# Kernel optimization log

Measured on AMD Instinct MI355X. Metric: run time of the kernel, lower is better.

Reference implementation:

```python
import jax, jax.numpy as jnp
import numpy as np

WS = 8
NUM_HEADS = 8
EMBED_DIM = 256
LN_EPS = 1e-5


def setup_inputs() -> dict:
    key = jax.random.key(0)
    ks = jax.random.split(key, 5)
    b, c, h, w = 4, EMBED_DIM, 128, 128
    return {
        "x": jax.random.normal(ks[0], (b, c, h, w), dtype=jnp.float32),
        "in_proj_w": jax.random.normal(ks[1], (3 * c, c), dtype=jnp.float32) * 0.02,
        "in_proj_b": jax.random.normal(ks[2], (3 * c,), dtype=jnp.float32) * 0.02,
        "out_w": jax.random.normal(ks[3], (c, c), dtype=jnp.float32) * 0.02,
        "out_b": jax.random.normal(ks[4], (c,), dtype=jnp.float32) * 0.02,
        "ln_w": jnp.ones((c,), dtype=jnp.float32),
        "ln_b": jnp.zeros((c,), dtype=jnp.float32),
    }


def reference(x, in_proj_w, in_proj_b, out_w, out_b, ln_w, ln_b):
    b, c, h, w = x.shape
    pad_h = (-h) % WS
    pad_w = (-w) % WS
    xp = jnp.pad(x, ((0, 0), (0, 0), (0, pad_h), (0, pad_w)))
    Hp, Wp = h + pad_h, w + pad_w
    h1, w1 = Hp // WS, Wp // WS
    L = h1 * w1            # attention sequence = number of windows
    N = b * WS * WS        # attention batch = b * within-window positions
    # rearrange 'b c (h1 h2) (w1 w2) -> (h1 w1) (b h2 w2) c', then batch-first
    t = xp.reshape(b, c, h1, WS, w1, WS)
    t = jnp.transpose(t, (2, 4, 0, 3, 5, 1)).reshape(L, N, c)
    t = jnp.transpose(t, (1, 0, 2))  # [N, L, c]
    # nn.MultiheadAttention (self-attention, no mask)
    qkv = t @ in_proj_w.T + in_proj_b  # [N, L, 3c]
    q, k, v = jnp.split(qkv, 3, axis=-1)
    D = c // NUM_HEADS
    q = q.reshape(N, L, NUM_HEADS, D) * (D ** -0.5)
    k = k.reshape(N, L, NUM_HEADS, D)
    v = v.reshape(N, L, NUM_HEADS, D)
    attn = jax.nn.softmax(jnp.einsum('nlhd,nmhd->nhlm', q, k), axis=-1)
    o = jnp.einsum('nhlm,nmhd->nlhd', attn, v).reshape(N, L, c)
    o = o @ out_w.T + out_b
    # LayerNorm over channel dim
    mu = jnp.mean(o, axis=-1, keepdims=True)
    var = jnp.mean(jnp.square(o - mu), axis=-1, keepdims=True)
    o = (o - mu) * jax.lax.rsqrt(var + LN_EPS) * ln_w + ln_b
    # inverse rearrange '(h1 w1) (b h2 w2) c -> b c (h1 h2) (w1 w2)'
    y = jnp.transpose(o, (1, 0, 2)).reshape(h1, w1, b, WS, WS, c)
    y = jnp.transpose(y, (2, 5, 0, 3, 1, 4)).reshape(b, c, Hp, Wp)
    return y[:, :, :h, :w]
```

## Files before the change

kernel.cpp:

```cpp
#include <hip/hip_runtime.h>
#include <stdint.h>
#include <stddef.h>


typedef __attribute__((ext_vector_type(8))) short bf16x8;
typedef __attribute__((ext_vector_type(4))) float f32x4;
typedef __attribute__((ext_vector_type(16))) float f32x16;
typedef __attribute__((ext_vector_type(4))) unsigned u32x4;
typedef unsigned short bf16u;

#define LOG2E 1.4426950408889634f
#define MFMA32(a, b, c) __builtin_amdgcn_mfma_f32_32x32x16_bf16(a, b, c, 0, 0, 0)

__device__ __forceinline__ bf16u f2b(float f) {
  uint32_t u = __float_as_uint(f);
  u += 0x7fffu + ((u >> 16) & 1u);
  return (bf16u)(u >> 16);
}
__device__ __forceinline__ float b2f(bf16u s) {
  return __uint_as_float(((uint32_t)s) << 16);
}

__device__ __forceinline__ void gload_lds16(const void* g, void* l) {
  __builtin_amdgcn_global_load_lds((__attribute__((address_space(1))) void*)(g),
                                   (__attribute__((address_space(3))) void*)(l),
                                   16, 0, 0);
}

__device__ __forceinline__ unsigned cvtpk(float a, float b) {
  unsigned r;
  asm("v_cvt_pk_bf16_f32 %0, %1, %2" : "=v"(r) : "v"(a), "v"(b));
  return r;
}

__device__ __forceinline__ void swap32(unsigned a, unsigned b, bool hi,
                                       unsigned& x, unsigned& y) {
#if __has_builtin(__builtin_amdgcn_permlane32_swap)
  typedef __attribute__((ext_vector_type(2))) unsigned uint2v;
  uint2v r = __builtin_amdgcn_permlane32_swap(a, b, false, false);
  x = r.x;
  y = r.y;
#else
  unsigned as = (unsigned)__shfl_xor((int)a, 32);
  unsigned bs = (unsigned)__shfl_xor((int)b, 32);
  x = hi ? bs : a;
  y = hi ? b : as;
#endif
}

__global__ __launch_bounds__(256) void k_convert(const float* __restrict__ s,
                                                 bf16u* __restrict__ d, int n) {
  int i = blockIdx.x * 256 + threadIdx.x;
  if (i < n) d[i] = f2b(s[i]);
}

__global__ __launch_bounds__(256) void k_rearrange(const float* __restrict__ x,
                                                   bf16u* __restrict__ Tb) {
  const int bid = blockIdx.x;
  const int ct = bid & 7, hh = (bid >> 3) & 127, b = bid >> 10;
  const int c0 = ct * 32;
  const int h1 = hh >> 3, h2 = hh & 7;
  __shared__ float tile[32][129];
  for (int e = threadIdx.x; e < 4096; e += 256) {
    int cc = e >> 7, ww = e & 127;
    tile[cc][ww] = x[(((size_t)(b * 256 + c0 + cc)) * 128 + hh) * 128 + ww];
  }
  __syncthreads();
  for (int e = threadIdx.x; e < 4096; e += 256) {
    int ww = e >> 5, cc = e & 31;
    int w1 = ww >> 3, w2 = ww & 7;
    int i = ((b * 64 + h2 * 8 + w2) << 8) | (h1 * 16 + w1);
    Tb[(size_t)i * 256 + c0 + cc] = f2b(tile[cc][ww]);
  }
}

__global__ __launch_bounds__(256) void k_qkv(const bf16u* __restrict__ Tb,
                                             const bf16u* __restrict__ Wb,
                                             const float* __restrict__ bias,
                                             bf16u* __restrict__ Qb,
                                             bf16u* __restrict__ Kb,
                                             bf16u* __restrict__ Vtb) {
  __shared__ bf16u As[128 * 32];
  __shared__ bf16u Bs[128 * 32];
  const int bid0 = blockIdx.x;
  const int bid = (bid0 & 7) * 384 + (bid0 >> 3);
  const int o0 = (bid % 6) * 128;
  const int i0 = (bid / 6) * 128;
  const int seg = o0 >> 8;
  const int t = threadIdx.x;
  const int lane = t & 63, lo = lane & 15, hi = lane >> 4;
  const int w = t >> 6, wr = w >> 1, wc = w & 1;
  const int srow = t >> 2, schunk = (t & 3) * 8, sbase = (t & 192) * 8;
  f32x4 acc[4][4] = {};
  for (int k0 = 0; k0 < 256; k0 += 32) {
    __syncthreads();
    gload_lds16(Tb + (size_t)(i0 + srow) * 256 + k0 + schunk, As + sbase);
    gload_lds16(Tb + (size_t)(i0 + 64 + srow) * 256 + k0 + schunk, As + 2048 + sbase);
    gload_lds16(Wb + (size_t)(o0 + srow) * 256 + k0 + schunk, Bs + sbase);
    gload_lds16(Wb + (size_t)(o0 + 64 + srow) * 256 + k0 + schunk, Bs + 2048 + sbase);
    __syncthreads();
    bf16x8 af[4], bf_[4];
#pragma unroll
    for (int m = 0; m < 4; ++m)
      af[m] = *(const bf16x8*)&As[(wr * 64 + m * 16 + lo) * 32 + hi * 8];
#pragma unroll
    for (int nn = 0; nn < 4; ++nn)
      bf_[nn] = *(const bf16x8*)&Bs[(wc * 64 + nn * 16 + lo) * 32 + hi * 8];
#pragma unroll
    for (int m = 0; m < 4; ++m)
#pragma unroll
      for (int nn = 0; nn < 4; ++nn)
        acc[m][nn] = __builtin_amdgcn_mfma_f32_16x16x32_bf16(af[m], bf_[nn], acc[m][nn], 0, 0, 0);
  }
  const float oscale = (seg == 0) ? (0.17677669529663687f * LOG2E) : 1.0f;
  bf16u* const dst = (seg == 0) ? Qb : (seg == 1 ? Kb : Vtb);
#pragma unroll
  for (int m = 0; m < 4; ++m) {
#pragma unroll
    for (int nn = 0; nn < 4; ++nn) {
      const int o = o0 + wc * 64 + nn * 16 + lo;
      const int within = o & 255, head = within >> 5, dd = within & 31;
      const float bia = bias[o];
#pragma unroll
      for (int r = 0; r < 4; ++r) {
        int tok = i0 + wr * 64 + m * 16 + hi * 4 + r;
        float v = (acc[m][nn][r] + bia) * oscale;
        int nt = tok >> 8, ls = tok & 255;
        size_t idx;
        if (seg == 2)
          idx = ((size_t)((nt * 8 + head) * 32 + dd)) * 256 + ls;
        else
          idx = ((size_t)((nt * 8 + head) * 256 + ls)) * 32 + dd;
        dst[idx] = f2b(v);
      }
    }
  }
}

__global__ __launch_bounds__(256, 2) void k_attn(const bf16u* __restrict__ Qb,
                                                 const bf16u* __restrict__ Kb,
                                                 const bf16u* __restrict__ Vtb,
                                                 bf16u* __restrict__ Ob) {
  const int nh = blockIdx.x;
  const int n = nh >> 3, h = nh & 7;
  const bf16u* Qp = Qb + (size_t)nh * 8192;
  const bf16u* Kp = Kb + (size_t)nh * 8192;
  const bf16u* Vp = Vtb + (size_t)nh * 8192;
  const int t = threadIdx.x, w = t >> 6, lane = t & 63;
  const int l31 = lane & 31;
  const bool hi5 = (lane & 32) != 0;

  bf16x8 qf[2][2];
#pragma unroll
  for (int qs = 0; qs < 2; ++qs)
#pragma unroll
    for (int dh = 0; dh < 2; ++dh)
      qf[qs][dh] = *(const bf16x8*)(Qp + (size_t)(w * 64 + qs * 32 + l31) * 32 +
                                    dh * 16 + (hi5 ? 8 : 0));

  const bf16u* kbase = Kp + (size_t)l31 * 32 + (hi5 ? 8 : 0);
  const bf16u* vbase = Vp + (size_t)l31 * 256 + (hi5 ? 8 : 0);

  bf16x8 kf0 = *(const bf16x8*)(kbase);
  bf16x8 kf1 = *(const bf16x8*)(kbase + 16);
  bf16x8 vf0 = *(const bf16x8*)(vbase);
  bf16x8 vf1 = *(const bf16x8*)(vbase + 16);

  f32x16 accO[2] = {};
  float rsum[2] = {0.f, 0.f};

#pragma unroll
  for (int kt = 0; kt < 8; ++kt) {
    const int nkt = (kt + 1) & 7;
    bf16x8 nk0 = *(const bf16x8*)(kbase + nkt * 1024);
    bf16x8 nk1 = *(const bf16x8*)(kbase + nkt * 1024 + 16);
    bf16x8 nv0 = *(const bf16x8*)(vbase + nkt * 32);
    bf16x8 nv1 = *(const bf16x8*)(vbase + nkt * 32 + 16);

#pragma unroll
    for (int qs = 0; qs < 2; ++qs) {
      f32x16 s = {};
      s = MFMA32(kf0, qf[qs][0], s);
      s = MFMA32(kf1, qf[qs][1], s);
      float ts0 = 0.f, ts1 = 0.f;
      unsigned pk[8];
#pragma unroll
      for (int jp = 0; jp < 8; ++jp) {
        float p0 = exp2f(s[2 * jp]);
        float p1 = exp2f(s[2 * jp + 1]);
        ts0 += p0;
        ts1 += p1;
        pk[jp] = cvtpk(p0, p1);
      }
      float ts = ts0 + ts1;
      ts += __shfl_xor(ts, 32);
      rsum[qs] += ts;
      unsigned x0, x1, x2, x3, y0, y1, y2, y3;
      swap32(pk[0], pk[2], hi5, x0, x2);
      swap32(pk[1], pk[3], hi5, x1, x3);
      swap32(pk[4], pk[6], hi5, y0, y2);
      swap32(pk[5], pk[7], hi5, y1, y3);
      u32x4 pa0 = {x0, x1, x2, x3};
      u32x4 pa1 = {y0, y1, y2, y3};
      accO[qs] = MFMA32(__builtin_bit_cast(bf16x8, pa0), vf0, accO[qs]);
      accO[qs] = MFMA32(__builtin_bit_cast(bf16x8, pa1), vf1, accO[qs]);
    }
    kf0 = nk0;
    kf1 = nk1;
    vf0 = nv0;
    vf1 = nv1;
  }
#pragma unroll
  for (int qs = 0; qs < 2; ++qs) {
    float rn = 1.0f / rsum[qs];
#pragma unroll
    for (int r = 0; r < 16; ++r) {
      int row = (r & 3) + 8 * (r >> 2) + ((lane & 32) >> 3);
      float c = __shfl(rn, (lane & 32) | row);
      float o = accO[qs][r] * c;
      Ob[((size_t)(n * 256 + w * 64 + qs * 32 + row)) * 256 + h * 32 + l31] = f2b(o);
    }
  }
}

__global__ __launch_bounds__(256) void k_out(const bf16u* __restrict__ Ob,
                                             const bf16u* __restrict__ Wb,
                                             const float* __restrict__ bias,
                                             const float* __restrict__ lnw,
                                             const float* __restrict__ lnb,
                                             bf16u* __restrict__ On) {
  __shared__ bf16u As[64 * 32];
  __shared__ bf16u Bs[256 * 32];
  __shared__ float red[64][4][2];
  const int i0 = blockIdx.x * 64;
  const int t = threadIdx.x, w = t >> 6, lane = t & 63, lo = lane & 15, hi = lane >> 4;
  const int srow = t >> 2, schunk = (t & 3) * 8, sbase = (t & 192) * 8;
  f32x4 acc[4][4] = {};
  for (int k0 = 0; k0 < 256; k0 += 32) {
    __syncthreads();
    gload_lds16(Ob + (size_t)(i0 + srow) * 256 + k0 + schunk, As + sbase);
#pragma unroll
    for (int j = 0; j < 4; ++j)
      gload_lds16(Wb + (size_t)(j * 64 + srow) * 256 + k0 + schunk, Bs + j * 2048 + sbase);
    __syncthreads();
    bf16x8 af[4], bf_[4];
#pragma unroll
    for (int m = 0; m < 4; ++m)
      af[m] = *(const bf16x8*)&As[(m * 16 + lo) * 32 + hi * 8];
#pragma unroll
    for (int nn = 0; nn < 4; ++nn)
      bf_[nn] = *(const bf16x8*)&Bs[(w * 64 + nn * 16 + lo) * 32 + hi * 8];
#pragma unroll
    for (int m = 0; m < 4; ++m)
#pragma unroll
      for (int nn = 0; nn < 4; ++nn)
        acc[m][nn] = __builtin_amdgcn_mfma_f32_16x16x32_bf16(af[m], bf_[nn], acc[m][nn], 0, 0, 0);
  }
#pragma unroll
  for (int m = 0; m < 4; ++m)
#pragma unroll
    for (int nn = 0; nn < 4; ++nn) {
      float bia = bias[w * 64 + nn * 16 + lo];
#pragma unroll
      for (int r = 0; r < 4; ++r) acc[m][nn][r] += bia;
    }
#pragma unroll
  for (int m = 0; m < 4; ++m)
#pragma unroll
    for (int r = 0; r < 4; ++r) {
      float sv = acc[m][0][r] + acc[m][1][r] + acc[m][2][r] + acc[m][3][r];
      float sq = acc[m][0][r] * acc[m][0][r] + acc[m][1][r] * acc[m][1][r] +
                 acc[m][2][r] * acc[m][2][r] + acc[m][3][r] * acc[m][3][r];
      sv += __shfl_xor(sv, 1); sq += __shfl_xor(sq, 1);
      sv += __shfl_xor(sv, 2); sq += __shfl_xor(sq, 2);
      sv += __shfl_xor(sv, 4); sq += __shfl_xor(sq, 4);
      sv += __shfl_xor(sv, 8); sq += __shfl_xor(sq, 8);
      if (lo == 0) {
        red[m * 16 + hi * 4 + r][w][0] = sv;
        red[m * 16 + hi * 4 + r][w][1] = sq;
      }
    }
  __syncthreads();
#pragma unroll
  for (int m = 0; m < 4; ++m)
#pragma unroll
    for (int r = 0; r < 4; ++r) {
      int row = m * 16 + hi * 4 + r;
      float S  = red[row][0][0] + red[row][1][0] + red[row][2][0] + red[row][3][0];
      float Q2 = red[row][0][1] + red[row][1][1] + red[row][2][1] + red[row][3][1];
      float mu = S * 0.00390625f;
      float var = Q2 * 0.00390625f - mu * mu;
      float rstd = rsqrtf(var + 1e-5f);
#pragma unroll
      for (int nn = 0; nn < 4; ++nn) {
        int oc = w * 64 + nn * 16 + lo;
        float o = (acc[m][nn][r] - mu) * rstd * lnw[oc] + lnb[oc];
        On[(size_t)(i0 + row) * 256 + oc] = f2b(o);
      }
    }
}

__global__ __launch_bounds__(256) void k_unrearrange(const bf16u* __restrict__ On,
                                                     float* __restrict__ y) {
  const int bid = blockIdx.x;
  const int ct = bid & 7, hh = (bid >> 3) & 127, b = bid >> 10;
  const int c0 = ct * 32;
  const int h1 = hh >> 3, h2 = hh & 7;
  __shared__ float tile[32][129];
  for (int e = threadIdx.x; e < 4096; e += 256) {
    int ww = e >> 5, cc = e & 31;
    int w1 = ww >> 3, w2 = ww & 7;
    int i = ((b * 64 + h2 * 8 + w2) << 8) | (h1 * 16 + w1);
    tile[cc][ww] = b2f(On[(size_t)i * 256 + c0 + cc]);
  }
  __syncthreads();
  for (int e = threadIdx.x; e < 4096; e += 256) {
    int cc = e >> 7, ww = e & 127;
    y[(((size_t)(b * 256 + c0 + cc)) * 128 + hh) * 128 + ww] = tile[cc][ww];
  }
}

extern "C" void kernel_launch(void* const* d_in, const int* in_sizes, int n_in,
                              void* d_out, int out_size, void* d_ws, size_t ws_size,
                              hipStream_t stream) {
  const float* x     = (const float*)d_in[0];
  const float* w_qkv = (const float*)d_in[1];
  const float* b_qkv = (const float*)d_in[2];
  const float* w_out = (const float*)d_in[3];
  const float* b_out = (const float*)d_in[4];
  const float* ln_w  = (const float*)d_in[5];
  const float* ln_b  = (const float*)d_in[6];
  float* y = (float*)d_out;

  const size_t SEG = 33554432;
  char* ws = (char*)d_ws;
  if (ws_size < 5 * SEG + 768 * 256 * 2 + 256 * 256 * 2) return;
  bf16u* Tb = (bf16u*)(ws);
  bf16u* Qb = (bf16u*)(ws + SEG);
  bf16u* Kb = (bf16u*)(ws + 2 * SEG);
  bf16u* Vtb = (bf16u*)(ws + 3 * SEG);
  bf16u* Ob = (bf16u*)(ws + 4 * SEG);
  bf16u* Wqkvb = (bf16u*)(ws + 5 * SEG);
  bf16u* Woutb = (bf16u*)(ws + 5 * SEG + 768 * 256 * 2);
  bf16u* On = Tb;

  k_convert<<<768, 256, 0, stream>>>(w_qkv, Wqkvb, 768 * 256);
  k_convert<<<256, 256, 0, stream>>>(w_out, Woutb, 256 * 256);
  k_rearrange<<<4096, 256, 0, stream>>>(x, Tb);
  k_qkv<<<3072, 256, 0, stream>>>(Tb, Wqkvb, b_qkv, Qb, Kb, Vtb);
  k_attn<<<2048, 256, 0, stream>>>(Qb, Kb, Vtb, Ob);
  k_out<<<1024, 256, 0, stream>>>(Ob, Woutb, b_out, ln_w, ln_b, On);
  k_unrearrange<<<4096, 256, 0, stream>>>(On, y);
}
```

Baseline: 209.4 us.

## Double K-tile depth, XOR-swizzle LDS layout, vectorize V-transpose stores in GEMMs

In the QKV and output-projection GEMMs, the K step per LDS stage doubles from 32 to 64. This halves the number of barrier-separated load/compute rounds. LDS rows become 64 elements wide with an XOR swizzle on the 16-byte chunk index, applied when filling via global_load_lds and when reading, to avoid bank conflicts. The V-transposed output in the QKV epilogue now writes four consecutive bf16 values as one packed 8-byte store instead of four scalar stores. LDS use per block grows, which may lower occupancy.

After: 179.9 us. -14.1%, faster.

```diff
diff --git a/kernel.cpp b/kernel.cpp
--- a/kernel.cpp
+++ b/kernel.cpp
@@ -7,6 +7,7 @@
 typedef __attribute__((ext_vector_type(4))) float f32x4;
 typedef __attribute__((ext_vector_type(16))) float f32x16;
 typedef __attribute__((ext_vector_type(4))) unsigned u32x4;
+typedef __attribute__((ext_vector_type(2))) unsigned u32x2;
 typedef unsigned short bf16u;
 
 #define LOG2E 1.4426950408889634f
@@ -80,8 +81,8 @@
                                              bf16u* __restrict__ Qb,
                                              bf16u* __restrict__ Kb,
                                              bf16u* __restrict__ Vtb) {
-  __shared__ bf16u As[128 * 32];
-  __shared__ bf16u Bs[128 * 32];
+  __shared__ bf16u As[128 * 64];
+  __shared__ bf16u Bs[128 * 64];
   const int bid0 = blockIdx.x;
   const int bid = (bid0 & 7) * 384 + (bid0 >> 3);
   const int o0 = (bid % 6) * 128;
@@ -90,30 +91,43 @@
   const int t = threadIdx.x;
   const int lane = t & 63, lo = lane & 15, hi = lane >> 4;
   const int w = t >> 6, wr = w >> 1, wc = w & 1;
-  const int srow = t >> 2, schunk = (t & 3) * 8, sbase = (t & 192) * 8;
+  const int rr = t >> 3, cc8 = t & 7;
   f32x4 acc[4][4] = {};
-  for (int k0 = 0; k0 < 256; k0 += 32) {
+  for (int k0 = 0; k0 < 256; k0 += 64) {
     __syncthreads();
-    gload_lds16(Tb + (size_t)(i0 + srow) * 256 + k0 + schunk, As + sbase);
-    gload_lds16(Tb + (size_t)(i0 + 64 + srow) * 256 + k0 + schunk, As + 2048 + sbase);
-    gload_lds16(Wb + (size_t)(o0 + srow) * 256 + k0 + schunk, Bs + sbase);
-    gload_lds16(Wb + (size_t)(o0 + 64 + srow) * 256 + k0 + schunk, Bs + 2048 + sbase);
+#pragma unroll
+    for (int j = 0; j < 4; ++j) {
+      const int row = j * 32 + rr;
+      const int sc = (cc8 ^ (row & 7)) * 8;
+      bf16u* const da = As + (j * 32 + w * 8) * 64;
+      bf16u* const db = Bs + (j * 32 + w * 8) * 64;
+      gload_lds16(Tb + (size_t)(i0 + row) * 256 + k0 + sc, da);
+      gload_lds16(Wb + (size_t)(o0 + row) * 256 + k0 + sc, db);
+    }
     __syncthreads();
-    bf16x8 af[4], bf_[4];
-#pragma unroll
-    for (int m = 0; m < 4; ++m)
-      af[m] = *(const bf16x8*)&As[(wr * 64 + m * 16 + lo) * 32 + hi * 8];
-#pragma unroll
-    for (int nn = 0; nn < 4; ++nn)
-      bf_[nn] = *(const bf16x8*)&Bs[(wc * 64 + nn * 16 + lo) * 32 + hi * 8];
-#pragma unroll
-    for (int m = 0; m < 4; ++m)
-#pragma unroll
-      for (int nn = 0; nn < 4; ++nn)
-        acc[m][nn] = __builtin_amdgcn_mfma_f32_16x16x32_bf16(af[m], bf_[nn], acc[m][nn], 0, 0, 0);
+#pragma unroll
+    for (int ks = 0; ks < 2; ++ks) {
+      bf16x8 af[4], bf_[4];
+#pragma unroll
+      for (int m = 0; m < 4; ++m) {
+        const int row = wr * 64 + m * 16 + lo;
+        const int c = (ks * 4 + hi) ^ (lo & 7);
+        af[m] = *(const bf16x8*)&As[row * 64 + c * 8];
+      }
+#pragma unroll
+      for (int nn = 0; nn < 4; ++nn) {
+        const int row = wc * 64 + nn * 16 + lo;
+        const int c = (ks * 4 + hi) ^ (lo & 7);
+        bf_[nn] = *(const bf16x8*)&Bs[row * 64 + c * 8];
+      }
+#pragma unroll
+      for (int m = 0; m < 4; ++m)
+#pragma unroll
+        for (int nn = 0; nn < 4; ++nn)
+          acc[m][nn] = __builtin_amdgcn_mfma_f32_16x16x32_bf16(af[m], bf_[nn], acc[m][nn], 0, 0, 0);
+    }
   }
   const float oscale = (seg == 0) ? (0.17677669529663687f * LOG2E) : 1.0f;
-  bf16u* const dst = (seg == 0) ? Qb : (seg == 1 ? Kb : Vtb);
 #pragma unroll
   for (int m = 0; m < 4; ++m) {
 #pragma unroll
@@ -121,17 +135,20 @@
       const int o = o0 + wc * 64 + nn * 16 + lo;
       const int within = o & 255, head = within >> 5, dd = within & 31;
       const float bia = bias[o];
-#pragma unroll
-      for (int r = 0; r < 4; ++r) {
-        int tok = i0 + wr * 64 + m * 16 + hi * 4 + r;
-        float v = (acc[m][nn][r] + bia) * oscale;
-        int nt = tok >> 8, ls = tok & 255;
-        size_t idx;
-        if (seg == 2)
-          idx = ((size_t)((nt * 8 + head) * 32 + dd)) * 256 + ls;
-        else
-          idx = ((size_t)((nt * 8 + head) * 256 + ls)) * 32 + dd;
-        dst[idx] = f2b(v);
+      const int tok0 = i0 + wr * 64 + m * 16 + hi * 4;
+      const int nt = tok0 >> 8, ls0 = tok0 & 255;
+      if (seg == 2) {
+        float v0 = acc[m][nn][0] + bia, v1 = acc[m][nn][1] + bia;
+        float v2 = acc[m][nn][2] + bia, v3 = acc[m][nn][3] + bia;
+        u32x2 pkd = {cvtpk(v0, v1), cvtpk(v2, v3)};
+        *(u32x2*)(Vtb + ((size_t)((nt * 8 + head) * 32 + dd)) * 256 + ls0) = pkd;
+      } else {
+        bf16u* const dst = (seg == 0) ? Qb : Kb;
+#pragma unroll
+        for (int r = 0; r < 4; ++r) {
+          float v = (acc[m][nn][r] + bia) * oscale;
+          dst[((size_t)((nt * 8 + head) * 256 + ls0 + r)) * 32 + dd] = f2b(v);
+        }
       }
     }
   }
@@ -229,32 +246,51 @@
                                              const float* __restrict__ lnw,
                                              const float* __restrict__ lnb,
                                              bf16u* __restrict__ On) {
-  __shared__ bf16u As[64 * 32];
-  __shared__ bf16u Bs[256 * 32];
+  __shared__ bf16u As[64 * 64];
+  __shared__ bf16u Bs[256 * 64];
   __shared__ float red[64][4][2];
   const int i0 = blockIdx.x * 64;
   const int t = threadIdx.x, w = t >> 6, lane = t & 63, lo = lane & 15, hi = lane >> 4;
-  const int srow = t >> 2, schunk = (t & 3) * 8, sbase = (t & 192) * 8;
+  const int rr = t >> 3, cc8 = t & 7;
   f32x4 acc[4][4] = {};
-  for (int k0 = 0; k0 < 256; k0 += 32) {
+  for (int k0 = 0; k0 < 256; k0 += 64) {
     __syncthreads();
-    gload_lds16(Ob + (size_t)(i0 + srow) * 256 + k0 + schunk, As + sbase);
-#pragma unroll
-    for (int j = 0; j < 4; ++j)
-      gload_lds16(Wb + (size_t)(j * 64 + srow) * 256 + k0 + schunk, Bs + j * 2048 + sbase);
+#pragma unroll
+    for (int j = 0; j < 2; ++j) {
+      const int row = j * 32 + rr;
+      const int sc = (cc8 ^ (row & 7)) * 8;
+      gload_lds16(Ob + (size_t)(i0 + row) * 256 + k0 + sc,
+                  As + (j * 32 + w * 8) * 64);
+    }
+#pragma unroll
+    for (int j = 0; j < 8; ++j) {
+      const int row = j * 32 + rr;
+      const int sc = (cc8 ^ (row & 7)) * 8;
+      gload_lds16(Wb + (size_t)row * 256 + k0 + sc,
+                  Bs + (j * 32 + w * 8) * 64);
+    }
     __syncthreads();
-    bf16x8 af[4], bf_[4];
-#pragma unroll
-    for (int m = 0; m < 4; ++m)
-      af[m] = *(const bf16x8*)&As[(m * 16 + lo) * 32 + hi * 8];
-#pragma unroll
-    for (int nn = 0; nn < 4; ++nn)
-      bf_[nn] = *(const bf16x8*)&Bs[(w * 64 + nn * 16 + lo) * 32 + hi * 8];
-#pragma unroll
-    for (int m = 0; m < 4; ++m)
-#pragma unroll
-      for (int nn = 0; nn < 4; ++nn)
-        acc[m][nn] = __builtin_amdgcn_mfma_f32_16x16x32_bf16(af[m], bf_[nn], acc[m][nn], 0, 0, 0);
+#pragma unroll
+    for (int ks = 0; ks < 2; ++ks) {
+      bf16x8 af[4], bf_[4];
+#pragma unroll
+      for (int m = 0; m < 4; ++m) {
+        const int row = m * 16 + lo;
+        const int c = (ks * 4 + hi) ^ (lo & 7);
+        af[m] = *(const bf16x8*)&As[row * 64 + c * 8];
+      }
+#pragma unroll
+      for (int nn = 0; nn < 4; ++nn) {
+        const int row = w * 64 + nn * 16 + lo;
+        const int c = (ks * 4 + hi) ^ (lo & 7);
+        bf_[nn] = *(const bf16x8*)&Bs[row * 64 + c * 8];
+      }
+#pragma unroll
+      for (int m = 0; m < 4; ++m)
+#pragma unroll
+        for (int nn = 0; nn < 4; ++nn)
+          acc[m][nn] = __builtin_amdgcn_mfma_f32_16x16x32_bf16(af[m], bf_[nn], acc[m][nn], 0, 0, 0);
+    }
   }
 #pragma unroll
   for (int m = 0; m < 4; ++m)
```
